# Optimization experiments

Hardware: AMD Instinct MI355X
Metric: run time of the kernel (lower is better)

The kernel has to match this reference:

```python
import jax, jax.numpy as jnp
import numpy as np

N_USER, N_MOVIE, H, E = 100000, 50000, 512, 500000

def setup_inputs() -> dict:
    key = jax.random.key(0)
    ks = jax.random.split(key, 8)
    z_user = jax.random.normal(ks[0], (N_USER, H), dtype=jnp.float32)
    z_movie = jax.random.normal(ks[1], (N_MOVIE, H), dtype=jnp.float32)
    edge_row = jax.random.randint(ks[2], (E,), 0, N_USER, dtype=jnp.int64)
    edge_col = jax.random.randint(ks[3], (E,), 0, N_MOVIE, dtype=jnp.int64)
    w1 = jax.random.normal(ks[4], (2 * H, H), dtype=jnp.float32) * (1.0 / np.sqrt(2 * H))
    b1 = jax.random.normal(ks[5], (H,), dtype=jnp.float32) * 0.01
    w2 = jax.random.normal(ks[6], (H, 1), dtype=jnp.float32) * (1.0 / np.sqrt(H))
    b2 = jax.random.normal(ks[7], (1,), dtype=jnp.float32) * 0.01
    return {"z_user": z_user, "z_movie": z_movie, "edge_row": edge_row,
            "edge_col": edge_col, "w1": w1, "b1": b1, "w2": w2, "b2": b2}

def reference(z_user, z_movie, edge_row, edge_col, w1, b1, w2, b2):
    # Gather endpoint embeddings and concat -> [E, 2H]
    z = jnp.concatenate([z_user[edge_row], z_movie[edge_col]], axis=-1)
    h = jax.nn.relu(z @ w1 + b1)      # [E, H]
    out = h @ w2 + b2                 # [E, 1]
    return out.reshape(-1)
```

## Files before the change

### kernel.cpp

```cpp
#include <hip/hip_runtime.h>
#include <hip/hip_bf16.h>

typedef __attribute__((ext_vector_type(8))) short bf16x8;
typedef __attribute__((ext_vector_type(4))) float f32x4;

#define HDIM 512
#define BM 128
#define BN 256
#define BK 64
#define BKP 72

__device__ __forceinline__ unsigned short f2bf(float f) {
  unsigned u = __float_as_uint(f);
  u += 0x7fffu + ((u >> 16) & 1u);
  return (unsigned short)(u >> 16);
}

__device__ __forceinline__ unsigned int pk_bf(float x, float y) {
  __hip_bfloat162 h = __float22bfloat162_rn(float2{x, y});
  union { __hip_bfloat162 b; unsigned int u; } cv; cv.b = h;
  return cv.u;
}

__global__ void k_w1t(const float* __restrict__ w1, unsigned short* __restrict__ w1t) {
  int idx = blockIdx.x * 256 + threadIdx.x;
  int k = idx >> 9;
  int n = idx & 511;
  w1t[n * 1024 + k] = f2bf(w1[idx]);
}

__global__ __launch_bounds__(512) void k_gemm(const float* __restrict__ A, int M,
    const unsigned short* __restrict__ w1t, int koff,
    unsigned short* __restrict__ C)
{
  __shared__ unsigned short As[BM][BKP];
  __shared__ unsigned short Bs[BN][BKP];
  const int tid  = threadIdx.x;
  const int lane = tid & 63;
  const int wid  = tid >> 6;
  const int wm = wid & 1, wn = wid >> 1;
  const int lm = lane & 15, lq = lane >> 4;
  const int nbase = blockIdx.x * BN;
  const int mbase = blockIdx.y * BM;

  f32x4 acc[4][4];
  #pragma unroll
  for (int i = 0; i < 4; ++i)
    #pragma unroll
    for (int j = 0; j < 4; ++j) acc[i][j] = (f32x4){0.f, 0.f, 0.f, 0.f};

  for (int kb = 0; kb < HDIM / BK; ++kb) {
    const int k0 = kb * BK;
    __syncthreads();
    #pragma unroll
    for (int i = 0; i < 4; ++i) {
      int fid = i * 512 + tid;
      int r = fid >> 4, c4 = fid & 15;
      int row = mbase + r; if (row > M - 1) row = M - 1;
      const float4 v = *(const float4*)&A[(size_t)row * HDIM + k0 + c4 * 4];
      unsigned int* dst = (unsigned int*)&As[r][c4 * 4];
      dst[0] = pk_bf(v.x, v.y);
      dst[1] = pk_bf(v.z, v.w);
    }
    #pragma unroll
    for (int i = 0; i < 4; ++i) {
      int cid = i * 512 + tid;
      int r = cid >> 3, c8 = cid & 7;
      const bf16x8 g = *(const bf16x8*)&w1t[(size_t)(nbase + r) * 1024 + koff + k0 + c8 * 8];
      *(bf16x8*)&Bs[r][c8 * 8] = g;
    }
    __syncthreads();
    #pragma unroll
    for (int ks = 0; ks < 2; ++ks) {
      bf16x8 af[4], bfr[4];
      #pragma unroll
      for (int t = 0; t < 4; ++t) {
        af[t]  = *(const bf16x8*)&As[wm * 64 + t * 16 + lm][ks * 32 + lq * 8];
        bfr[t] = *(const bf16x8*)&Bs[wn * 64 + t * 16 + lm][ks * 32 + lq * 8];
      }
      #pragma unroll
      for (int mi = 0; mi < 4; ++mi)
        #pragma unroll
        for (int ni = 0; ni < 4; ++ni)
          acc[mi][ni] = __builtin_amdgcn_mfma_f32_16x16x32_bf16(af[mi], bfr[ni], acc[mi][ni], 0, 0, 0);
    }
  }
  #pragma unroll
  for (int mi = 0; mi < 4; ++mi)
    #pragma unroll
    for (int ni = 0; ni < 4; ++ni)
      #pragma unroll
      for (int r = 0; r < 4; ++r) {
        int rg = mbase + wm * 64 + mi * 16 + lq * 4 + r;
        int cg = nbase + wn * 64 + ni * 16 + lm;
        if (rg < M) C[(size_t)rg * HDIM + cg] = f2bf(acc[mi][ni][r]);
      }
}

__global__ __launch_bounds__(256) void k_edge(const int* __restrict__ er, const int* __restrict__ ec,
    const unsigned short* __restrict__ u1, const unsigned short* __restrict__ m1,
    const float* __restrict__ b1, const float* __restrict__ w2, const float* __restrict__ b2,
    float* __restrict__ out, int E)
{
  const int lane = threadIdx.x & 63;
  const int gwid = blockIdx.x * 4 + (threadIdx.x >> 6);
  const int nw   = gridDim.x * 4;
  const float4 b1a = *(const float4*)&b1[lane * 8];
  const float4 b1b = *(const float4*)&b1[lane * 8 + 4];
  const float4 w2a = *(const float4*)&w2[lane * 8];
  const float4 w2b = *(const float4*)&w2[lane * 8 + 4];
  const float bias2 = b2[0];
  for (int e = gwid * 2; e < E; e += nw * 2) {
    const int r0 = er[e], c0 = ec[e];
    const int r1 = er[e + 1], c1 = ec[e + 1];
    const uint4 ua0 = *(const uint4*)&u1[(size_t)r0 * HDIM + lane * 8];
    const uint4 va0 = *(const uint4*)&m1[(size_t)c0 * HDIM + lane * 8];
    const uint4 ua1 = *(const uint4*)&u1[(size_t)r1 * HDIM + lane * 8];
    const uint4 va1 = *(const uint4*)&m1[(size_t)c1 * HDIM + lane * 8];
    float p0 = 0.f, p1 = 0.f, s;
    s = __uint_as_float(ua0.x << 16)        + __uint_as_float(va0.x << 16)        + b1a.x; s = fmaxf(s, 0.f); p0 += s * w2a.x;
    s = __uint_as_float(ua0.x & 0xffff0000u)+ __uint_as_float(va0.x & 0xffff0000u)+ b1a.y; s = fmaxf(s, 0.f); p0 += s * w2a.y;
    s = __uint_as_float(ua0.y << 16)        + __uint_as_float(va0.y << 16)        + b1a.z; s = fmaxf(s, 0.f); p0 += s * w2a.z;
    s = __uint_as_float(ua0.y & 0xffff0000u)+ __uint_as_float(va0.y & 0xffff0000u)+ b1a.w; s = fmaxf(s, 0.f); p0 += s * w2a.w;
    s = __uint_as_float(ua0.z << 16)        + __uint_as_float(va0.z << 16)        + b1b.x; s = fmaxf(s, 0.f); p0 += s * w2b.x;
    s = __uint_as_float(ua0.z & 0xffff0000u)+ __uint_as_float(va0.z & 0xffff0000u)+ b1b.y; s = fmaxf(s, 0.f); p0 += s * w2b.y;
    s = __uint_as_float(ua0.w << 16)        + __uint_as_float(va0.w << 16)        + b1b.z; s = fmaxf(s, 0.f); p0 += s * w2b.z;
    s = __uint_as_float(ua0.w & 0xffff0000u)+ __uint_as_float(va0.w & 0xffff0000u)+ b1b.w; s = fmaxf(s, 0.f); p0 += s * w2b.w;
    s = __uint_as_float(ua1.x << 16)        + __uint_as_float(va1.x << 16)        + b1a.x; s = fmaxf(s, 0.f); p1 += s * w2a.x;
    s = __uint_as_float(ua1.x & 0xffff0000u)+ __uint_as_float(va1.x & 0xffff0000u)+ b1a.y; s = fmaxf(s, 0.f); p1 += s * w2a.y;
    s = __uint_as_float(ua1.y << 16)        + __uint_as_float(va1.y << 16)        + b1a.z; s = fmaxf(s, 0.f); p1 += s * w2a.z;
    s = __uint_as_float(ua1.y & 0xffff0000u)+ __uint_as_float(va1.y & 0xffff0000u)+ b1a.w; s = fmaxf(s, 0.f); p1 += s * w2a.w;
    s = __uint_as_float(ua1.z << 16)        + __uint_as_float(va1.z << 16)        + b1b.x; s = fmaxf(s, 0.f); p1 += s * w2b.x;
    s = __uint_as_float(ua1.z & 0xffff0000u)+ __uint_as_float(va1.z & 0xffff0000u)+ b1b.y; s = fmaxf(s, 0.f); p1 += s * w2b.y;
    s = __uint_as_float(ua1.w << 16)        + __uint_as_float(va1.w << 16)        + b1b.z; s = fmaxf(s, 0.f); p1 += s * w2b.z;
    s = __uint_as_float(ua1.w & 0xffff0000u)+ __uint_as_float(va1.w & 0xffff0000u)+ b1b.w; s = fmaxf(s, 0.f); p1 += s * w2b.w;
    #pragma unroll
    for (int off = 32; off > 0; off >>= 1) {
      p0 += __shfl_down(p0, off, 64);
      p1 += __shfl_down(p1, off, 64);
    }
    if (lane == 0) *(float2*)&out[e] = float2{p0 + bias2, p1 + bias2};
  }
}

__global__ __launch_bounds__(256) void k_fallback(const float* __restrict__ zu, const float* __restrict__ zm,
    const int* __restrict__ er, const int* __restrict__ ec, const float* __restrict__ w1,
    const float* __restrict__ b1, const float* __restrict__ w2, const float* __restrict__ b2,
    float* __restrict__ out, int E)
{
  __shared__ float Zs[64][33];
  __shared__ float Ws[32][65];
  __shared__ float outacc[64];
  __shared__ int ridx[64], cidx[64];
  const int tid = threadIdx.x;
  const int ebase = blockIdx.x * 64;
  if (tid < 64) {
    int e = ebase + tid; if (e > E - 1) e = E - 1;
    ridx[tid] = er[e]; cidx[tid] = ec[e];
    outacc[tid] = 0.f;
  }
  const int tx = tid & 15, ty = tid >> 4;
  for (int nt = 0; nt < 8; ++nt) {
    float acc[4][4] = {};
    for (int kc = 0; kc < 32; ++kc) {
      __syncthreads();
      #pragma unroll
      for (int i = 0; i < 8; ++i) {
        int id = i * 256 + tid;
        int rr = id >> 5, cc = id & 31;
        int k = kc * 32 + cc;
        Zs[rr][cc] = (k < 512) ? zu[(size_t)ridx[rr] * 512 + k]
                               : zm[(size_t)cidx[rr] * 512 + (k - 512)];
      }
      #pragma unroll
      for (int i = 0; i < 8; ++i) {
        int id = i * 256 + tid;
        int kk = id >> 6, nn = id & 63;
        Ws[kk][nn] = w1[(size_t)(kc * 32 + kk) * 512 + nt * 64 + nn];
      }
      __syncthreads();
      #pragma unroll
      for (int kk = 0; kk < 32; ++kk) {
        float a0 = Zs[ty*4+0][kk], a1 = Zs[ty*4+1][kk], a2 = Zs[ty*4+2][kk], a3 = Zs[ty*4+3][kk];
        float q0 = Ws[kk][tx*4+0], q1 = Ws[kk][tx*4+1], q2 = Ws[kk][tx*4+2], q3 = Ws[kk][tx*4+3];
        acc[0][0] += a0*q0; acc[0][1] += a0*q1; acc[0][2] += a0*q2; acc[0][3] += a0*q3;
        acc[1][0] += a1*q0; acc[1][1] += a1*q1; acc[1][2] += a1*q2; acc[1][3] += a1*q3;
        acc[2][0] += a2*q0; acc[2][1] += a2*q1; acc[2][2] += a2*q2; acc[2][3] += a2*q3;
        acc[3][0] += a3*q0; acc[3][1] += a3*q1; acc[3][2] += a3*q2; acc[3][3] += a3*q3;
      }
    }
    #pragma unroll
    for (int i = 0; i < 4; ++i) {
      float p = 0.f;
      #pragma unroll
      for (int j = 0; j < 4; ++j) {
        int n = nt * 64 + tx * 4 + j;
        float h = acc[i][j] + b1[n]; h = fmaxf(h, 0.f);
        p += h * w2[n];
      }
      atomicAdd(&outacc[ty * 4 + i], p);
    }
  }
  __syncthreads();
  if (tid < 64 && (ebase + tid) < E) out[ebase + tid] = outacc[tid] + b2[0];
}

extern "C" void kernel_launch(void* const* d_in, const int* in_sizes, int n_in,
                              void* d_out, int out_size, void* d_ws, size_t ws_size,
                              hipStream_t stream)
{
  const float* z_user  = (const float*)d_in[0];
  const float* z_movie = (const float*)d_in[1];
  const int*   erow    = (const int*)d_in[2];
  const int*   ecol    = (const int*)d_in[3];
  const float* w1      = (const float*)d_in[4];
  const float* b1      = (const float*)d_in[5];
  const float* w2      = (const float*)d_in[6];
  const float* b2      = (const float*)d_in[7];
  float* out = (float*)d_out;

  const int NU = in_sizes[0] / HDIM;
  const int NM = in_sizes[1] / HDIM;
  const int E  = in_sizes[2];

  const size_t need = ((size_t)NU * HDIM + (size_t)NM * HDIM + (size_t)1024 * 512) * 2;
  if (ws_size >= need) {
    unsigned short* u1  = (unsigned short*)d_ws;
    unsigned short* m1  = u1 + (size_t)NU * HDIM;
    unsigned short* w1t = m1 + (size_t)NM * HDIM;
    k_w1t<<<(1024 * 512) / 256, 256, 0, stream>>>(w1, w1t);
    k_gemm<<<dim3(HDIM / BN, (NU + BM - 1) / BM), 512, 0, stream>>>(z_user,  NU, w1t, 0,   u1);
    k_gemm<<<dim3(HDIM / BN, (NM + BM - 1) / BM), 512, 0, stream>>>(z_movie, NM, w1t, 512, m1);
    k_edge<<<2048, 256, 0, stream>>>(erow, ecol, u1, m1, b1, w2, b2, out, E);
  } else {
    k_fallback<<<(E + 63) / 64, 256, 0, stream>>>(z_user, z_movie, erow, ecol, w1, b1, w2, b2, out, E);
  }
}
```

Baseline: 594.6 us.

## Group edges by movie via counting sort to reuse movie rows in edge kernel

```diff
diff --git a/kernel.cpp b/kernel.cpp
--- a/kernel.cpp
+++ b/kernel.cpp
@@ -22,11 +22,61 @@
   return cv.u;
 }
 
-__global__ void k_w1t(const float* __restrict__ w1, unsigned short* __restrict__ w1t) {
+__global__ void k_w1t(const float* __restrict__ w1, unsigned short* __restrict__ w1t,
+                      int* __restrict__ cnt, int nzero) {
   int idx = blockIdx.x * 256 + threadIdx.x;
   int k = idx >> 9;
   int n = idx & 511;
   w1t[n * 1024 + k] = f2bf(w1[idx]);
+  if (idx < nzero) cnt[idx] = 0;
+}
+
+__global__ void k_hist(const int* __restrict__ ec, int* __restrict__ cnt, int E) {
+  int e = blockIdx.x * 256 + threadIdx.x;
+  if (e < E) atomicAdd(&cnt[ec[e]], 1);
+}
+
+__global__ __launch_bounds__(1024) void k_scan(const int* __restrict__ cnt, int* __restrict__ ptr,
+                                               int* __restrict__ cur, int n) {
+  __shared__ int wsum[16];
+  __shared__ int carry_s;
+  const int tid = threadIdx.x, lane = tid & 63, w = tid >> 6;
+  if (tid == 0) carry_s = 0;
+  __syncthreads();
+  for (int base = 0; base < n; base += 1024) {
+    int i = base + tid;
+    int x = (i < n) ? cnt[i] : 0;
+    int v = x;
+    #pragma unroll
+    for (int off = 1; off < 64; off <<= 1) {
+      int t = __shfl_up(v, off, 64);
+      if (lane >= off) v += t;
+    }
+    if (lane == 63) wsum[w] = v;
+    __syncthreads();
+    int wpre = 0;
+    #pragma unroll
+    for (int j = 0; j < 16; ++j) { int s = wsum[j]; if (j < w) wpre += s; }
+    int carry = carry_s;
+    __syncthreads();
+    int incl = v + wpre;
+    if (i < n) { int excl = carry + incl - x; ptr[i] = excl; cur[i] = excl; }
+    if (tid == 1023) carry_s = carry + incl;
+    __syncthreads();
+  }
+  if (threadIdx.x == 0) ptr[n] = carry_s;
+}
+
+__global__ void k_scatter(const int* __restrict__ er, const int* __restrict__ ec,
+                          int* __restrict__ cur, int* __restrict__ srow,
+                          int* __restrict__ seid, int E) {
+  int e = blockIdx.x * 256 + threadIdx.x;
+  if (e < E) {
+    int c = ec[e];
+    int pos = atomicAdd(&cur[c], 1);
+    srow[pos] = er[e];
+    seid[pos] = e;
+  }
 }
 
 __global__ __launch_bounds__(512) void k_gemm(const float* __restrict__ A, int M,
@@ -97,6 +147,73 @@
       }
 }
 
+__device__ __forceinline__ float edot(const uint4 ua, const float* vb, const float* wv) {
+  float p = 0.f, s;
+  s = __uint_as_float(ua.x << 16)         + vb[0]; s = fmaxf(s, 0.f); p += s * wv[0];
+  s = __uint_as_float(ua.x & 0xffff0000u) + vb[1]; s = fmaxf(s, 0.f); p += s * wv[1];
+  s = __uint_as_float(ua.y << 16)         + vb[2]; s = fmaxf(s, 0.f); p += s * wv[2];
+  s = __uint_as_float(ua.y & 0xffff0000u) + vb[3]; s = fmaxf(s, 0.f); p += s * wv[3];
+  s = __uint_as_float(ua.z << 16)         + vb[4]; s = fmaxf(s, 0.f); p += s * wv[4];
+  s = __uint_as_float(ua.z & 0xffff0000u) + vb[5]; s = fmaxf(s, 0.f); p += s * wv[5];
+  s = __uint_as_float(ua.w << 16)         + vb[6]; s = fmaxf(s, 0.f); p += s * wv[6];
+  s = __uint_as_float(ua.w & 0xffff0000u) + vb[7]; s = fmaxf(s, 0.f); p += s * wv[7];
+  return p;
+}
+
+__global__ __launch_bounds__(256) void k_edge_g(const int* __restrict__ ptr,
+    const int* __restrict__ srow, const int* __restrict__ seid,
+    const unsigned short* __restrict__ u1, const unsigned short* __restrict__ m1,
+    const float* __restrict__ b1, const float* __restrict__ w2, const float* __restrict__ b2,
+    float* __restrict__ out, int nmov)
+{
+  const int lane = threadIdx.x & 63;
+  const int gw = blockIdx.x * 4 + (threadIdx.x >> 6);
+  const int nw = gridDim.x * 4;
+  const float4 b1a = *(const float4*)&b1[lane * 8];
+  const float4 b1b = *(const float4*)&b1[lane * 8 + 4];
+  const float4 w2a = *(const float4*)&w2[lane * 8];
+  const float4 w2b = *(const float4*)&w2[lane * 8 + 4];
+  float wv[8] = {w2a.x, w2a.y, w2a.z, w2a.w, w2b.x, w2b.y, w2b.z, w2b.w};
+  const float bias2 = b2[0];
+  for (int c = gw; c < nmov; c += nw) {
+    const int beg = ptr[c], end = ptr[c + 1];
+    if (beg == end) continue;
+    const uint4 va = *(const uint4*)&m1[(size_t)c * HDIM + lane * 8];
+    float vb[8];
+    vb[0] = __uint_as_float(va.x << 16)         + b1a.x;
+    vb[1] = __uint_as_float(va.x & 0xffff0000u) + b1a.y;
+    vb[2] = __uint_as_float(va.y << 16)         + b1a.z;
+    vb[3] = __uint_as_float(va.y & 0xffff0000u) + b1a.w;
+    vb[4] = __uint_as_float(va.z << 16)         + b1b.x;
+    vb[5] = __uint_as_float(va.z & 0xffff0000u) + b1b.y;
+    vb[6] = __uint_as_float(va.w << 16)         + b1b.z;
+    vb[7] = __uint_as_float(va.w & 0xffff0000u) + b1b.w;
+    int i = beg;
+    for (; i + 1 < end; i += 2) {
+      const int r0 = srow[i], r1 = srow[i + 1];
+      const int e0 = seid[i], e1 = seid[i + 1];
+      const uint4 ua0 = *(const uint4*)&u1[(size_t)r0 * HDIM + lane * 8];
+      const uint4 ua1 = *(const uint4*)&u1[(size_t)r1 * HDIM + lane * 8];
+      float p0 = edot(ua0, vb, wv);
+      float p1 = edot(ua1, vb, wv);
+      #pragma unroll
+      for (int off = 32; off > 0; off >>= 1) {
+        p0 += __shfl_down(p0, off, 64);
+        p1 += __shfl_down(p1, off, 64);
+      }
+      if (lane == 0) { out[e0] = p0 + bias2; out[e1] = p1 + bias2; }
+    }
+    if (i < end) {
+      const int r0 = srow[i], e0 = seid[i];
+      const uint4 ua0 = *(const uint4*)&u1[(size_t)r0 * HDIM + lane * 8];
+      float p0 = edot(ua0, vb, wv);
+      #pragma unroll
+      for (int off = 32; off > 0; off >>= 1) p0 += __shfl_down(p0, off, 64);
+      if (lane == 0) out[e0] = p0 + bias2;
+    }
+  }
+}
+
 __global__ __launch_bounds__(256) void k_edge(const int* __restrict__ er, const int* __restrict__ ec,
     const unsigned short* __restrict__ u1, const unsigned short* __restrict__ m1,
     const float* __restrict__ b1, const float* __restrict__ w2, const float* __restrict__ b2,
@@ -109,37 +226,26 @@
   const float4 b1b = *(const float4*)&b1[lane * 8 + 4];
   const float4 w2a = *(const float4*)&w2[lane * 8];
   const float4 w2b = *(const float4*)&w2[lane * 8 + 4];
+  float bv[8] = {b1a.x, b1a.y, b1a.z, b1a.w, b1b.x, b1b.y, b1b.z, b1b.w};
+  float wv[8] = {w2a.x, w2a.y, w2a.z, w2a.w, w2b.x, w2b.y, w2b.z, w2b.w};
   const float bias2 = b2[0];
-  for (int e = gwid * 2; e < E; e += nw * 2) {
-    const int r0 = er[e], c0 = ec[e];
-    const int r1 = er[e + 1], c1 = ec[e + 1];
-    const uint4 ua0 = *(const uint4*)&u1[(size_t)r0 * HDIM + lane * 8];
-    const uint4 va0 = *(const uint4*)&m1[(size_t)c0 * HDIM + lane * 8];
-    const uint4 ua1 = *(const uint4*)&u1[(size_t)r1 * HDIM + lane * 8];
-    const uint4 va1 = *(const uint4*)&m1[(size_t)c1 * HDIM + lane * 8];
-    float p0 = 0.f, p1 = 0.f, s;
-    s = __uint_as_float(ua0.x << 16)        + __uint_as_float(va0.x << 16)        + b1a.x; s = fmaxf(s, 0.f); p0 += s * w2a.x;
-    s = __uint_as_float(ua0.x & 0xffff0000u)+ __uint_as_float(va0.x & 0xffff0000u)+ b1a.y; s = fmaxf(s, 0.f); p0 += s * w2a.y;
-    s = __uint_as_float(ua0.y << 16)        + __uint_as_float(va0.y << 16)        + b1a.z; s = fmaxf(s, 0.f); p0 += s * w2a.z;
-    s = __uint_as_float(ua0.y & 0xffff0000u)+ __uint_as_float(va0.y & 0xffff0000u)+ b1a.w; s = fmaxf(s, 0.f); p0 += s * w2a.w;
-    s = __uint_as_float(ua0.z << 16)        + __uint_as_float(va0.z << 16)        + b1b.x; s = fmaxf(s, 0.f); p0 += s * w2b.x;
-    s = __uint_as_float(ua0.z & 0xffff0000u)+ __uint_as_float(va0.z & 0xffff0000u)+ b1b.y; s = fmaxf(s, 0.f); p0 += s * w2b.y;
-    s = __uint_as_float(ua0.w << 16)        + __uint_as_float(va0.w << 16)        + b1b.z; s = fmaxf(s, 0.f); p0 += s * w2b.z;
-    s = __uint_as_float(ua0.w & 0xffff0000u)+ __uint_as_float(va0.w & 0xffff0000u)+ b1b.w; s = fmaxf(s, 0.f); p0 += s * w2b.w;
-    s = __uint_as_float(ua1.x << 16)        + __uint_as_float(va1.x << 16)        + b1a.x; s = fmaxf(s, 0.f); p1 += s * w2a.x;
-    s = __uint_as_float(ua1.x & 0xffff0000u)+ __uint_as_float(va1.x & 0xffff0000u)+ b1a.y; s = fmaxf(s, 0.f); p1 += s * w2a.y;
-    s = __uint_as_float(ua1.y << 16)        + __uint_as_float(va1.y << 16)        + b1a.z; s = fmaxf(s, 0.f); p1 += s * w2a.z;
-    s = __uint_as_float(ua1.y & 0xffff0000u)+ __uint_as_float(va1.y & 0xffff0000u)+ b1a.w; s = fmaxf(s, 0.f); p1 += s * w2a.w;
-    s = __uint_as_float(ua1.z << 16)        + __uint_as_float(va1.z << 16)        + b1b.x; s = fmaxf(s, 0.f); p1 += s * w2b.x;
-    s = __uint_as_float(ua1.z & 0xffff0000u)+ __uint_as_float(va1.z & 0xffff0000u)+ b1b.y; s = fmaxf(s, 0.f); p1 += s * w2b.y;
-    s = __uint_as_float(ua1.w << 16)        + __uint_as_float(va1.w << 16)        + b1b.z; s = fmaxf(s, 0.f); p1 += s * w2b.z;
-    s = __uint_as_float(ua1.w & 0xffff0000u)+ __uint_as_float(va1.w & 0xffff0000u)+ b1b.w; s = fmaxf(s, 0.f); p1 += s * w2b.w;
-    #pragma unroll
-    for (int off = 32; off > 0; off >>= 1) {
-      p0 += __shfl_down(p0, off, 64);
-      p1 += __shfl_down(p1, off, 64);
-    }
-    if (lane == 0) *(float2*)&out[e] = float2{p0 + bias2, p1 + bias2};
+  for (int e = gwid; e < E; e += nw) {
+    const int r = er[e], c = ec[e];
+    const uint4 ua = *(const uint4*)&u1[(size_t)r * HDIM + lane * 8];
+    const uint4 va = *(const uint4*)&m1[(size_t)c * HDIM + lane * 8];
+    float vb[8];
+    vb[0] = __uint_as_float(va.x << 16)         + bv[0];
+    vb[1] = __uint_as_float(va.x & 0xffff0000u) + bv[1];
+    vb[2] = __uint_as_float(va.y << 16)         + bv[2];
+    vb[3] = __uint_as_float(va.y & 0xffff0000u) + bv[3];
+    vb[4] = __uint_as_float(va.z << 16)         + bv[4];
+    vb[5] = __uint_as_float(va.z & 0xffff0000u) + bv[5];
+    vb[6] = __uint_as_float(va.w << 16)         + bv[6];
+    vb[7] = __uint_as_float(va.w & 0xffff0000u) + bv[7];
+    float p = edot(ua, vb, wv);
+    #pragma unroll
+    for (int off = 32; off > 0; off >>= 1) p += __shfl_down(p, off, 64);
+    if (lane == 0) out[e] = p + bias2;
   }
 }
 
@@ -223,15 +329,33 @@
   const int NM = in_sizes[1] / HDIM;
   const int E  = in_sizes[2];
 
-  const size_t need = ((size_t)NU * HDIM + (size_t)NM * HDIM + (size_t)1024 * 512) * 2;
-  if (ws_size >= need) {
+  const size_t shorts = (size_t)(NU + NM) * HDIM + (size_t)1024 * 512;
+  const size_t need_basic  = shorts * 2;
+  const size_t need_sorted = shorts * 2 + ((size_t)3 * NM + 1 + (size_t)2 * E) * 4;
+
+  if (ws_size >= need_basic) {
     unsigned short* u1  = (unsigned short*)d_ws;
     unsigned short* m1  = u1 + (size_t)NU * HDIM;
     unsigned short* w1t = m1 + (size_t)NM * HDIM;
-    k_w1t<<<(1024 * 512) / 256, 256, 0, stream>>>(w1, w1t);
-    k_gemm<<<dim3(HDIM / BN, (NU + BM - 1) / BM), 512, 0, stream>>>(z_user,  NU, w1t, 0,   u1);
-    k_gemm<<<dim3(HDIM / BN, (NM + BM - 1) / BM), 512, 0, stream>>>(z_movie, NM, w1t, 512, m1);
-    k_edge<<<2048, 256, 0, stream>>>(erow, ecol, u1, m1, b1, w2, b2, out, E);
+    if (ws_size >= need_sorted) {
+      int* cnt  = (int*)(w1t + (size_t)1024 * 512);
+      int* ptr  = cnt + NM;
+      int* cur  = ptr + NM + 1;
+      int* srow = cur + NM;
+      int* seid = srow + E;
+      k_w1t<<<(1024 * 512) / 256, 256, 0, stream>>>(w1, w1t, cnt, NM);
+      k_hist<<<(E + 255) / 256, 256, 0, stream>>>(ecol, cnt, E);
+      k_scan<<<1, 1024, 0, stream>>>(cnt, ptr, cur, NM);
+      k_scatter<<<(E + 255) / 256, 256, 0, stream>>>(erow, ecol, cur, srow, seid, E);
+      k_gemm<<<dim3(HDIM / BN, (NU + BM - 1) / BM), 512, 0, stream>>>(z_user,  NU, w1t, 0,   u1);
+      k_gemm<<<dim3(HDIM / BN, (NM + BM - 1) / BM), 512, 0, stream>>>(z_movie, NM, w1t, 512, m1);
+      k_edge_g<<<2048, 256, 0, stream>>>(ptr, srow, seid, u1, m1, b1, w2, b2, out, NM);
+    } else {
+      k_w1t<<<(1024 * 512) / 256, 256, 0, stream>>>(w1, w1t, (int*)d_ws, 0);
+      k_gemm<<<dim3(HDIM / BN, (NU + BM - 1) / BM), 512, 0, stream>>>(z_user,  NU, w1t, 0,   u1);
+      k_gemm<<<dim3(HDIM / BN, (NM + BM - 1) / BM), 512, 0, stream>>>(z_movie, NM, w1t, 512, m1);
+      k_edge<<<2048, 256, 0, stream>>>(erow, ecol, u1, m1, b1, w2, b2, out, E);
+    }
   } else {
     k_fallback<<<(E + 63) / 64, 256, 0, stream>>>(z_user, z_movie, erow, ecol, w1, b1, w2, b2, out, E);
   }
```

After: 643.2 us. +8.2%, slower.
